# Optimization experiments

Hardware: AMD Instinct MI355X
Metric: run time of the kernel (lower is better)

Reference implementation:

```python
import jax, jax.numpy as jnp
import numpy as np
from jax import lax

EPS = 1e-10

def _ln(x, g, b):
    m = x.mean(-1, keepdims=True)
    v = x.var(-1, keepdims=True)
    return (x - m) / jnp.sqrt(v + 1e-5) * g + b

def _gather(t, idx):
    # t: (B, HW, c), idx: (B, HW, d) -> (B, HW, d, c); out[n,i,k,:] = t[n, idx[n,i,k], :]
    return jax.vmap(lambda tn, In: tn[In])(t, idx)

def setup_inputs() -> dict:
    key = jax.random.key(0)
    ks = jax.random.split(key, 20)
    b, v, c, d, h, w, hid, ksz = 2, 2, 128, 64, 64, 64, 256, 5
    hw = h * w
    Bf = b * v  # v_1 == 1 target view per reference view
    std = 0.02
    return {
        'features_mv': jax.random.normal(ks[0], (b, v, c, h, w), jnp.float32),
        'warp_indices': jax.random.randint(ks[1], (Bf, hw, d), 0, hw, jnp.int32),
        'depth_prob': jax.random.uniform(ks[2], (Bf, hw, d), jnp.float32),
        'ln1_g': jnp.ones((c,), jnp.float32), 'ln1_b': jnp.zeros((c,), jnp.float32),
        'wq': jax.random.normal(ks[3], (c, c), jnp.float32) * std, 'bq': jnp.zeros((c,), jnp.float32),
        'wk': jax.random.normal(ks[4], (c, c), jnp.float32) * std, 'bk': jnp.zeros((c,), jnp.float32),
        'wv': jax.random.normal(ks[5], (c, c), jnp.float32) * std, 'bv': jnp.zeros((c,), jnp.float32),
        'k_pe': jax.random.normal(ks[6], (1, 1, d), jnp.float32) * std,
        'v_pe': jax.random.normal(ks[7], (1, 1, d), jnp.float32) * std,
        'rpe': jax.random.normal(ks[8], (1, 1, d), jnp.float32) * std,
        'proj_w': jax.random.normal(ks[9], (c, c), jnp.float32) * std, 'proj_b': jnp.zeros((c,), jnp.float32),
        'ln2_g': jnp.ones((c,), jnp.float32), 'ln2_b': jnp.zeros((c,), jnp.float32),
        'fc1_w': jax.random.normal(ks[10], (c, hid), jnp.float32) * std, 'fc1_b': jnp.zeros((hid,), jnp.float32),
        'dw_w': jax.random.normal(ks[11], (hid, 1, ksz, ksz), jnp.float32) * std, 'dw_b': jnp.zeros((hid,), jnp.float32),
        'fc2_w': jax.random.normal(ks[12], (hid, c), jnp.float32) * std, 'fc2_b': jnp.zeros((c,), jnp.float32),
    }

def reference(features_mv, warp_indices, depth_prob, ln1_g, ln1_b, wq, bq, wk, bk, wv, bv,
              k_pe, v_pe, rpe, proj_w, proj_b, ln2_g, ln2_b, fc1_w, fc1_b, dw_w, dw_b, fc2_w, fc2_b):
    b, v, c, h, w = features_mv.shape
    hw = h * w
    hid = fc1_w.shape[1]
    scale = c ** (-0.5)  # num_heads = 1 -> head_dim = dim

    # (b v) (h w) c
    x = features_mv.reshape(b * v, c, hw).transpose(0, 2, 1)
    shortcut = x
    xn = _ln(x, ln1_g, ln1_b)
    q = xn @ wq + bq
    k = xn @ wk + bk
    vv = xn @ wv + bv

    # nn pairing: v=2, v_1=1 -> each reference view attends the other view
    Q = (q.reshape(b, v, hw, c) * scale).reshape(b * v, hw, c)
    K = k.reshape(b, v, hw, c)[:, ::-1].reshape(b * v, hw, c)
    V = vv.reshape(b, v, hw, c)[:, ::-1].reshape(b * v, hw, c)

    # SMM_QmK: cost[n,i,k] = sum_c Q[n,i,c] * K[n, idx[n,i,k], c]
    Kg = _gather(K, warp_indices)                       # (B, hw, d, c)
    cost = jnp.einsum('bic,bikc->bik', Q, Kg)
    Q_pe = Q.sum(-1, keepdims=True)                     # (B, hw, 1)
    cost = cost + Q_pe * k_pe + rpe                     # broadcast (1,1,d)

    # (Sim_UNet similarity refinement omitted: UNetModel source unavailable; identity here)
    attn = jax.nn.softmax(cost, axis=-1)
    attn = attn * depth_prob
    attn = (attn + EPS) / (attn.sum(-1, keepdims=True) + EPS)

    # SMM_AmV: out[n,i,c] = sum_k attn[n,i,k] * V[n, idx[n,i,k], c]
    Vg = _gather(V, warp_indices)                       # (B, hw, d, c)
    out = jnp.einsum('bik,bikc->bic', attn, Vg)
    out = out + (attn * v_pe).sum(-1, keepdims=True)

    # projection + residual (v_1 == 1 so B == b*v)
    x = shortcut + (out @ proj_w + proj_b)

    # ConvFFN residual branch
    xn2 = _ln(x, ln2_g, ln2_b)
    y = jax.nn.gelu(xn2 @ fc1_w + fc1_b, approximate=False)
    yi = y.transpose(0, 2, 1).reshape(b * v, hid, h, w)
    yc = lax.conv_general_dilated(yi, dw_w, (1, 1), 'SAME', feature_group_count=hid,
                                  dimension_numbers=('NCHW', 'OIHW', 'NCHW'))
    yc = jax.nn.gelu(yc + dw_b[None, :, None, None], approximate=False)
    y = y + yc.reshape(b * v, hid, hw).transpose(0, 2, 1)
    y = y @ fc2_w + fc2_b
    return x + y
```

## Files before the change

### kernel.cpp

```cpp
#include <hip/hip_runtime.h>
#include <math.h>

#define TOK   16384
#define HW    4096
#define C     128
#define D     64
#define HID   256

constexpr float LN_EPS = 1e-5f;
constexpr float EPS_R  = 1e-10f;
constexpr float QSCALE = 0.08838834764831845f;

typedef __attribute__((ext_vector_type(8))) short  bf16x8;
typedef __attribute__((ext_vector_type(4))) float  f32x4;
typedef __attribute__((ext_vector_type(2))) _Float16 half2v;
#define MFMA16(a, b, c) __builtin_amdgcn_mfma_f32_16x16x32_bf16((a), (b), (c), 0, 0, 0)

__device__ __forceinline__ float bflo(unsigned u) { return __uint_as_float(u << 16); }
__device__ __forceinline__ float bfhi(unsigned u) { return __uint_as_float(u & 0xffff0000u); }
__device__ __forceinline__ unsigned short f2bf(float f) {
  unsigned u = __float_as_uint(f);
  unsigned r = (u + 0x7fffu + ((u >> 16) & 1u)) >> 16;
  return (unsigned short)r;
}
__device__ __forceinline__ unsigned short f2h(float f) {
  _Float16 h = (_Float16)f;
  unsigned short r;
  __builtin_memcpy(&r, &h, 2);
  return r;
}
__device__ __forceinline__ float gelu_exact(float x) {
  return 0.5f * x * (1.0f + erff(x * 0.7071067811865476f));
}

union U4H { uint4 v; half2v h[4]; };
union U1H { unsigned v; half2v h; };

#if __has_builtin(__builtin_amdgcn_fdot2)
__device__ __forceinline__ float dot2h(half2v a, half2v b, float c) {
  return __builtin_amdgcn_fdot2(a, b, c, false);
}
#else
__device__ __forceinline__ float dot2h(half2v a, half2v b, float c) {
  return c + (float)a.x * (float)b.x + (float)a.y * (float)b.y;
}
#endif

__global__ __launch_bounds__(256) void k_prepln1(const float* __restrict__ wq,
    const float* __restrict__ wk, const float* __restrict__ wv,
    const float* __restrict__ pw, const float* __restrict__ f1w,
    const float* __restrict__ f2w, unsigned short* __restrict__ wt,
    const float* __restrict__ feat, const float* __restrict__ g,
    const float* __restrict__ b, unsigned short* __restrict__ xnb) {
  __shared__ float tile[32][C + 1];
  int bidx = blockIdx.x;
  if (bidx < 512) {
    int id = bidx * 256 + threadIdx.x;
    if (id < 16384) {
      int n = id >> 7, k = id & 127;
      wt[id] = f2bf(wq[k * 128 + n]);
    } else if (id < 32768) {
      int e = id - 16384; int n = e >> 7, k = e & 127;
      wt[id] = f2bf(wk[k * 128 + n]);
    } else if (id < 49152) {
      int e = id - 32768; int n = e >> 7, k = e & 127;
      wt[id] = f2bf(wv[k * 128 + n]);
    } else if (id < 65536) {
      int e = id - 49152; int n = e >> 7, k = e & 127;
      wt[id] = f2bf(pw[k * 128 + n]);
    } else if (id < 98304) {
      int e = id - 65536; int n = e >> 7, k = e & 127;
      wt[id] = f2bf(f1w[k * 256 + n]);
    } else {
      int e = id - 98304; int n = e >> 8, k = e & 255;
      wt[id] = f2bf(f2w[k * 128 + n]);
    }
    return;
  }
  int t0 = (bidx - 512) * 32;
  int n = t0 / HW, i0 = t0 % HW;
  int tid = threadIdx.x;
  const float* fb = feat + (size_t)n * C * HW;
  for (int e = tid; e < 32 * C; e += 256) {
    int ch = e >> 5, ii = e & 31;
    tile[ii][ch] = fb[(size_t)ch * HW + i0 + ii];
  }
  __syncthreads();
  int wave = tid >> 6, lane = tid & 63;
  for (int tkn = wave; tkn < 32; tkn += 4) {
    float a0 = tile[tkn][lane];
    float a1 = tile[tkn][lane + 64];
    float s = a0 + a1;
    for (int off = 32; off; off >>= 1) s += __shfl_xor(s, off, 64);
    float mean = s * (1.0f / 128.0f);
    float d0 = a0 - mean, d1 = a1 - mean;
    float v = d0 * d0 + d1 * d1;
    for (int off = 32; off; off >>= 1) v += __shfl_xor(v, off, 64);
    float rstd = rsqrtf(v * (1.0f / 128.0f) + LN_EPS);
    size_t ro = (size_t)(t0 + tkn) * C;
    xnb[ro + lane]      = f2bf(d0 * rstd * g[lane] + b[lane]);
    xnb[ro + lane + 64] = f2bf(d1 * rstd * g[lane + 64] + b[lane + 64]);
  }
}

__global__ __launch_bounds__(256) void k_qkv(const unsigned short* __restrict__ xnb,
    const unsigned short* __restrict__ wt,
    const float* __restrict__ bq, const float* __restrict__ bk,
    const float* __restrict__ bv, unsigned short* __restrict__ qh,
    unsigned short* __restrict__ ksw, unsigned short* __restrict__ vsw) {
  int w = threadIdx.x >> 6, lane = threadIdx.x & 63;
  int q4 = lane >> 4, m = lane & 15;
  int t0 = blockIdx.x * 64 + w * 16;
  int wsel = blockIdx.y >> 1;
  int hf = blockIdx.y & 1;
  const unsigned short* Wt = wt + wsel * 16384;
  const unsigned short* ap = xnb + (size_t)(t0 + m) * C + q4 * 8;
  bf16x8 a[4];
  #pragma unroll
  for (int ks = 0; ks < 4; ks++) a[ks] = *(const bf16x8*)(ap + ks * 32);
  f32x4 acc[4];
  #pragma unroll
  for (int nt = 0; nt < 4; nt++) acc[nt] = (f32x4){0.f, 0.f, 0.f, 0.f};
  #pragma unroll
  for (int nt = 0; nt < 4; nt++) {
    const unsigned short* bp = Wt + (size_t)(hf * 64 + nt * 16 + m) * C + q4 * 8;
    #pragma unroll
    for (int ks = 0; ks < 4; ks++) {
      bf16x8 bfrag = *(const bf16x8*)(bp + ks * 32);
      acc[nt] = MFMA16(a[ks], bfrag, acc[nt]);
    }
  }
  const float* B = (wsel == 0) ? bq : ((wsel == 1) ? bk : bv);
  float sc = (wsel == 0) ? QSCALE : 1.0f;
  unsigned short* O = (wsel == 0) ? qh : ((wsel == 1) ? ksw : vsw);
  int n = t0 >> 12, i0 = t0 & 4095;
  int base = (wsel == 0) ? t0 : (((n ^ 1) << 12) + i0);
  #pragma unroll
  for (int nt = 0; nt < 4; nt++) {
    int col = hf * 64 + nt * 16 + m;
    float bb = B[col];
    #pragma unroll
    for (int reg = 0; reg < 4; reg++) {
      int row = base + q4 * 4 + reg;
      O[(size_t)row * C + col] = f2h((acc[nt][reg] + bb) * sc);
    }
  }
}

__global__ __launch_bounds__(256, 3) void k_attn_proj_fc1(
    const unsigned short* __restrict__ qh, const unsigned short* __restrict__ ksw,
    const unsigned short* __restrict__ vsw, const int* __restrict__ widx,
    const float* __restrict__ dprob, const float* __restrict__ kpe,
    const float* __restrict__ vpe, const float* __restrict__ rpe,
    const unsigned short* __restrict__ wt, const float* __restrict__ pb,
    const float* __restrict__ feat, float* __restrict__ xio,
    const float* __restrict__ g2, const float* __restrict__ b2,
    const float* __restrict__ f1b, unsigned short* __restrict__ y) {
  __shared__ unsigned short axn[16 * C];
  __shared__ float ps1[4][16];
  __shared__ float ps2[4][16];
  int lane = threadIdx.x & 63;
  int wave = threadIdx.x >> 6;
  int bid = blockIdx.x;
  int n = (bid >> 1) & 3;
  int within = ((bid >> 3) << 1) | (bid & 1);
  int T0 = n * HW + within * 16;
  const unsigned short* Kb = ksw + (size_t)n * HW * C;
  const unsigned short* Vb = vsw + (size_t)n * HW * C;
  int gg = lane >> 3, s = lane & 7;
  half2v ones = {(_Float16)1.0f, (_Float16)1.0f};

  for (int tj = 0; tj < 4; ++tj) {
    int token = T0 + wave * 4 + tj;
    int myidx = widx[(size_t)token * D + lane];
    float mydp = dprob[(size_t)token * D + lane];
    half2v qreg[8];
    {
      const unsigned short* qp = qh + (size_t)token * C + s * 16;
      U4H qa, qb2;
      qa.v = *(const uint4*)(qp);
      qb2.v = *(const uint4*)(qp + 8);
      #pragma unroll
      for (int i = 0; i < 4; i++) { qreg[i] = qa.h[i]; qreg[4 + i] = qb2.h[i]; }
    }
    int rowv[8];
    #pragma unroll
    for (int pass = 0; pass < 8; ++pass)
      rowv[pass] = __shfl(myidx, pass * 8 + gg, 64);
    uint4 ka[8], kb[8];
    #pragma unroll
    for (int pass = 0; pass < 8; ++pass) {
      const unsigned short* kr = Kb + (size_t)rowv[pass] * C + s * 16;
      ka[pass] = *(const uint4*)(kr);
      kb[pass] = *(const uint4*)(kr + 8);
    }
    unsigned vv0[32];
    #pragma unroll
    for (int j = 0; j < 32; j++) {
      int row = __builtin_amdgcn_readlane(myidx, j);
      vv0[j] = *(const unsigned*)(Vb + (size_t)row * C + lane * 2);
    }
    float qpe = 0.f;
    #pragma unroll
    for (int i = 0; i < 8; i++) qpe = dot2h(qreg[i], ones, qpe);
    qpe += __shfl_xor(qpe, 1, 64);
    qpe += __shfl_xor(qpe, 2, 64);
    qpe += __shfl_xor(qpe, 4, 64);
    float mycost = 0.f;
    #pragma unroll
    for (int pass = 0; pass < 8; ++pass) {
      U4H ua, ub;
      ua.v = ka[pass]; ub.v = kb[pass];
      float p = 0.f;
      #pragma unroll
      for (int i = 0; i < 4; i++) p = dot2h(ua.h[i], qreg[i], p);
      #pragma unroll
      for (int i = 0; i < 4; i++) p = dot2h(ub.h[i], qreg[4 + i], p);
      p += __shfl_xor(p, 1, 64);
      p += __shfl_xor(p, 2, 64);
      p += __shfl_xor(p, 4, 64);
      float t = __shfl(p, (lane & 7) << 3, 64);
      if (pass == gg) mycost = t;
    }
    mycost += qpe * kpe[lane] + rpe[lane];
    float mx = mycost;
    for (int off = 32; off; off >>= 1) mx = fmaxf(mx, __shfl_xor(mx, off, 64));
    float e = __expf(mycost - mx);
    float ssum = e;
    for (int off = 32; off; off >>= 1) ssum += __shfl_xor(ssum, off, 64);
    float attn = (e / ssum) * mydp;
    float s2 = attn;
    for (int off = 32; off; off >>= 1) s2 += __shfl_xor(s2, off, 64);
    attn = (attn + EPS_R) / (s2 + EPS_R);
    float vpt = attn * vpe[lane];
    for (int off = 32; off; off >>= 1) vpt += __shfl_xor(vpt, off, 64);
    float o0 = vpt, o1 = vpt;
    unsigned att_u = __float_as_uint(attn);
    unsigned vv1[32];
    #pragma unroll
    for (int j = 0; j < 32; j++) {
      int row = __builtin_amdgcn_readlane(myidx, 32 + j);
      vv1[j] = *(const unsigned*)(Vb + (size_t)row * C + lane * 2);
    }
    #pragma unroll
    for (int j = 0; j < 32; j++) {
      float a = __uint_as_float(__builtin_amdgcn_readlane(att_u, j));
      U1H h; h.v = vv0[j];
      o0 += a * (float)h.h.x;
      o1 += a * (float)h.h.y;
    }
    #pragma unroll
    for (int j = 0; j < 32; j++) {
      float a = __uint_as_float(__builtin_amdgcn_readlane(att_u, 32 + j));
      U1H h; h.v = vv1[j];
      o0 += a * (float)h.h.x;
      o1 += a * (float)h.h.y;
    }
    unsigned pk = (unsigned)f2bf(o0) | ((unsigned)f2bf(o1) << 16);
    int row = wave * 4 + tj;
    int boff = row * 256 + lane * 4;
    boff ^= (row & 15) << 4;
    *(unsigned*)((char*)axn + boff) = pk;
  }
  __syncthreads();

  int q4 = lane >> 4, m = lane & 15;
  bf16x8 a[4];
  #pragma unroll
  for (int ks = 0; ks < 4; ks++) {
    int boff = m * 256 + ks * 64 + q4 * 16;
    boff ^= m << 4;
    a[ks] = *(const bf16x8*)((char*)axn + boff);
  }
  const unsigned short* Wp = wt + 3 * 16384;
  f32x4 acc[2];
  #pragma unroll
  for (int nt = 0; nt < 2; nt++) acc[nt] = (f32x4){0.f, 0.f, 0.f, 0.f};
  #pragma unroll
  for (int nt = 0; nt < 2; nt++) {
    int colt = wave * 32 + nt * 16;
    const unsigned short* bp = Wp + (size_t)(colt + m) * C + q4 * 8;
    #pragma unroll
    for (int ks = 0; ks < 4; ks++) {
      bf16x8 bfrag = *(const bf16x8*)(bp + ks * 32);
      acc[nt] = MFMA16(a[ks], bfrag, acc[nt]);
    }
  }
  int ibase = (T0 & 4095) + q4 * 4;
  float s1[4] = {0.f, 0.f, 0.f, 0.f}, s2b[4] = {0.f, 0.f, 0.f, 0.f};
  #pragma unroll
  for (int nt = 0; nt < 2; nt++) {
    int col = wave * 32 + nt * 16 + m;
    float bb = pb[col];
    const float* fp = feat + ((size_t)n * C + col) * HW + ibase;
    #pragma unroll
    for (int reg = 0; reg < 4; reg++) {
      float v = acc[nt][reg] + bb + fp[reg];
      acc[nt][reg] = v;
      s1[reg] += v;
      s2b[reg] += v * v;
    }
  }
  #pragma unroll
  for (int reg = 0; reg < 4; reg++) {
    #pragma unroll
    for (int off = 1; off < 16; off <<= 1) {
      s1[reg] += __shfl_xor(s1[reg], off, 64);
      s2b[reg] += __shfl_xor(s2b[reg], off, 64);
    }
  }
  if (m == 0) {
    #pragma unroll
    for (int reg = 0; reg < 4; reg++) {
      ps1[wave][q4 * 4 + reg] = s1[reg];
      ps2[wave][q4 * 4 + reg] = s2b[reg];
    }
  }
  __syncthreads();
  float mean[4], rstd[4];
  #pragma unroll
  for (int reg = 0; reg < 4; reg++) {
    int row = q4 * 4 + reg;
    float t1 = ps1[0][row] + ps1[1][row] + ps1[2][row] + ps1[3][row];
    float t2 = ps2[0][row] + ps2[1][row] + ps2[2][row] + ps2[3][row];
    mean[reg] = t1 * (1.0f / 128.0f);
    float var = t2 * (1.0f / 128.0f) - mean[reg] * mean[reg];
    rstd[reg] = rsqrtf(var + LN_EPS);
  }
  #pragma unroll
  for (int nt = 0; nt < 2; nt++) {
    int col = wave * 32 + nt * 16 + m;
    float gc = g2[col], bc = b2[col];
    #pragma unroll
    for (int reg = 0; reg < 4; reg++) {
      int row = q4 * 4 + reg;
      float v = acc[nt][reg];
      xio[(size_t)(T0 + row) * C + col] = v;
      unsigned short xv = f2bf((v - mean[reg]) * rstd[reg] * gc + bc);
      int boff = row * 256 + col * 2;
      boff ^= (row & 15) << 4;
      *(unsigned short*)((char*)axn + boff) = xv;
    }
  }
  __syncthreads();

  bf16x8 af[4];
  #pragma unroll
  for (int ks = 0; ks < 4; ks++) {
    int boff = m * 256 + ks * 64 + q4 * 16;
    boff ^= m << 4;
    af[ks] = *(const bf16x8*)((char*)axn + boff);
  }
  const unsigned short* Wf = wt + 65536;
  f32x4 acc2[4];
  #pragma unroll
  for (int nt = 0; nt < 4; nt++) acc2[nt] = (f32x4){0.f, 0.f, 0.f, 0.f};
  #pragma unroll
  for (int nt = 0; nt < 4; nt++) {
    int colt = wave * 64 + nt * 16;
    const unsigned short* bp = Wf + (size_t)(colt + m) * C + q4 * 8;
    #pragma unroll
    for (int ks = 0; ks < 4; ks++) {
      bf16x8 bfrag = *(const bf16x8*)(bp + ks * 32);
      acc2[nt] = MFMA16(af[ks], bfrag, acc2[nt]);
    }
  }
  #pragma unroll
  for (int nt = 0; nt < 4; nt++) {
    int col = wave * 64 + nt * 16 + m;
    float bb = f1b[col];
    #pragma unroll
    for (int reg = 0; reg < 4; reg++) {
      int row = T0 + q4 * 4 + reg;
      y[(size_t)row * HID + col] = f2bf(gelu_exact(acc2[nt][reg] + bb));
    }
  }
}

__global__ __launch_bounds__(256) void k_dwconv(const unsigned short* __restrict__ y,
    const float* __restrict__ w, const float* __restrict__ bias,
    unsigned short* __restrict__ ysum) {
  __shared__ float tile[8][401];
  __shared__ float wl[8][25];
  __shared__ float bl[8];
  __shared__ unsigned short outl[256][8];
  int bid = blockIdx.x;
  int tile_id = bid & 15;
  int cb = (bid >> 4) & 31;
  int n = bid >> 9;
  int ty = (tile_id >> 2) * 16, tx = (tile_id & 3) * 16;
  int ch0 = cb * 8;
  int tid = threadIdx.x;
  if (tid < 200) wl[tid / 25][tid % 25] = w[(size_t)(ch0 + tid / 25) * 25 + tid % 25];
  if (tid < 8) bl[tid] = bias[ch0 + tid];
  const unsigned short* yb = y + (size_t)n * HW * HID;
  for (int p = tid; p < 400; p += 256) {
    int py = p / 20, px = p % 20;
    int gy = ty + py - 2, gx = tx + px - 2;
    uint4 v = make_uint4(0u, 0u, 0u, 0u);
    if (gy >= 0 && gy < 64 && gx >= 0 && gx < 64)
      v = *(const uint4*)(yb + (size_t)(gy * 64 + gx) * HID + ch0);
    tile[0][p] = bflo(v.x); tile[1][p] = bfhi(v.x);
    tile[2][p] = bflo(v.y); tile[3][p] = bfhi(v.y);
    tile[4][p] = bflo(v.z); tile[5][p] = bfhi(v.z);
    tile[6][p] = bflo(v.w); tile[7][p] = bfhi(v.w);
  }
  __syncthreads();
  int cc = tid & 7;
  int xx = (tid >> 3) & 15;
  int yg = tid >> 7;
  float wreg[25];
  #pragma unroll
  for (int k = 0; k < 25; k++) wreg[k] = wl[cc][k];
  float bb = bl[cc];
  float win[12][5];
  #pragma unroll
  for (int r = 0; r < 12; r++)
    #pragma unroll
    for (int dx = 0; dx < 5; dx++)
      win[r][dx] = tile[cc][(yg * 8 + r) * 20 + xx + dx];
  #pragma unroll
  for (int j = 0; j < 8; ++j) {
    float acc = 0.f;
    #pragma unroll
    for (int dy = 0; dy < 5; ++dy)
      #pragma unroll
      for (int dx = 0; dx < 5; ++dx)
        acc += wreg[dy * 5 + dx] * win[j + dy][dx];
    float o = win[j + 2][2] + gelu_exact(acc + bb);
    int yy = yg * 8 + j;
    outl[yy * 16 + xx][cc] = f2bf(o);
  }
  __syncthreads();
  {
    int p = tid;
    int yy = p >> 4, xx2 = p & 15;
    uint4 val = *(const uint4*)outl[p];
    *(uint4*)(ysum + (size_t)(n * HW + (ty + yy) * 64 + tx + xx2) * HID + ch0) = val;
  }
}

__global__ __launch_bounds__(256) void k_fc2(const unsigned short* __restrict__ ysum,
    const unsigned short* __restrict__ wt, const float* __restrict__ f2b,
    const float* __restrict__ xio, float* __restrict__ outp) {
  int w = threadIdx.x >> 6, lane = threadIdx.x & 63;
  int q4 = lane >> 4, m = lane & 15;
  int t0 = blockIdx.x * 64 + w * 16;
  int quarter = blockIdx.y;
  const unsigned short* Wt = wt + 98304;
  const unsigned short* ap = ysum + (size_t)(t0 + m) * HID + q4 * 8;
  bf16x8 a[8];
  #pragma unroll
  for (int ks = 0; ks < 8; ks++) a[ks] = *(const bf16x8*)(ap + ks * 32);
  f32x4 acc[2];
  #pragma unroll
  for (int nt = 0; nt < 2; nt++) acc[nt] = (f32x4){0.f, 0.f, 0.f, 0.f};
  #pragma unroll
  for (int nt = 0; nt < 2; nt++) {
    const unsigned short* bp = Wt + (size_t)(quarter * 32 + nt * 16 + m) * HID + q4 * 8;
    #pragma unroll
    for (int ks = 0; ks < 8; ks++) {
      bf16x8 bfrag = *(const bf16x8*)(bp + ks * 32);
      acc[nt] = MFMA16(a[ks], bfrag, acc[nt]);
    }
  }
  #pragma unroll
  for (int nt = 0; nt < 2; nt++) {
    int col = quarter * 32 + nt * 16 + m;
    float bb = f2b[col];
    #pragma unroll
    for (int reg = 0; reg < 4; reg++) {
      int row = t0 + q4 * 4 + reg;
      outp[(size_t)row * C + col] = acc[nt][reg] + bb + xio[(size_t)row * C + col];
    }
  }
}

extern "C" void kernel_launch(void* const* d_in, const int* in_sizes, int n_in,
                              void* d_out, int out_size, void* d_ws, size_t ws_size,
                              hipStream_t stream) {
  (void)in_sizes; (void)n_in; (void)out_size; (void)ws_size;
  const float* feat  = (const float*)d_in[0];
  const int*   widx  = (const int*)d_in[1];
  const float* dprob = (const float*)d_in[2];
  const float* ln1g  = (const float*)d_in[3];
  const float* ln1b  = (const float*)d_in[4];
  const float* wq    = (const float*)d_in[5];
  const float* bq    = (const float*)d_in[6];
  const float* wk    = (const float*)d_in[7];
  const float* bk    = (const float*)d_in[8];
  const float* wv    = (const float*)d_in[9];
  const float* bv    = (const float*)d_in[10];
  const float* kpe   = (const float*)d_in[11];
  const float* vpe   = (const float*)d_in[12];
  const float* rpe   = (const float*)d_in[13];
  const float* pw    = (const float*)d_in[14];
  const float* pb    = (const float*)d_in[15];
  const float* ln2g  = (const float*)d_in[16];
  const float* ln2b  = (const float*)d_in[17];
  const float* f1w   = (const float*)d_in[18];
  const float* f1b   = (const float*)d_in[19];
  const float* dww   = (const float*)d_in[20];
  const float* dwb   = (const float*)d_in[21];
  const float* f2w   = (const float*)d_in[22];
  const float* f2b   = (const float*)d_in[23];

  float* ws = (float*)d_ws;
  const size_t M2 = (size_t)TOK * C;
  float* xio = ws;
  unsigned short* qhb   = (unsigned short*)(ws + M2);
  unsigned short* xnb   = (unsigned short*)(ws + M2 + M2 / 2);
  unsigned short* ksb   = (unsigned short*)(ws + 2 * M2);
  unsigned short* vsb   = (unsigned short*)(ws + 2 * M2 + M2 / 2);
  unsigned short* yb    = (unsigned short*)(ws + 3 * M2);
  unsigned short* ysumb = (unsigned short*)(ws + 4 * M2);
  unsigned short* wtb   = (unsigned short*)(ws + 5 * M2);

  k_prepln1<<<1024, 256, 0, stream>>>(wq, wk, wv, pw, f1w, f2w, wtb,
                                      feat, ln1g, ln1b, xnb);
  k_qkv    <<<dim3(TOK / 64, 6), 256, 0, stream>>>(xnb, wtb, bq, bk, bv, qhb, ksb, vsb);
  k_attn_proj_fc1<<<TOK / 16, 256, 0, stream>>>(qhb, ksb, vsb, widx, dprob, kpe, vpe,
                                                rpe, wtb, pb, feat, xio, ln2g, ln2b,
                                                f1b, yb);
  k_dwconv <<<2048, 256, 0, stream>>>(yb, dww, dwb, ysumb);
  k_fc2    <<<dim3(TOK / 64, 4), 256, 0, stream>>>(ysumb, wtb, f2b, xio, (float*)d_out);
}
```

Measured before the change: 201.2 us.

## Fuse LayerNorm1 into QKV projection and widen attention blocks to 512 threads

Splits the weight-prep kernel from LayerNorm1 and fuses LayerNorm1 directly into the QKV GEMM. Each 16-token block normalizes into a swizzled shared-memory tile and computes all three projections there, so the bf16 normalized intermediate is no longer written to and re-read from global memory. The attention/proj/fc1 kernel now uses 512-thread blocks: eight waves each handle two tokens, and the projection and fc1 column work is split eight ways. The QKV GEMM now runs with only 1024 blocks of 16 tokens, and the larger attention blocks may change occupancy and register pressure.

```diff
diff --git a/kernel.cpp b/kernel.cpp
--- a/kernel.cpp
+++ b/kernel.cpp
@@ -46,50 +46,53 @@
 }
 #endif
 
-__global__ __launch_bounds__(256) void k_prepln1(const float* __restrict__ wq,
+__global__ __launch_bounds__(256) void k_prep(const float* __restrict__ wq,
     const float* __restrict__ wk, const float* __restrict__ wv,
     const float* __restrict__ pw, const float* __restrict__ f1w,
-    const float* __restrict__ f2w, unsigned short* __restrict__ wt,
-    const float* __restrict__ feat, const float* __restrict__ g,
-    const float* __restrict__ b, unsigned short* __restrict__ xnb) {
-  __shared__ float tile[32][C + 1];
-  int bidx = blockIdx.x;
-  if (bidx < 512) {
-    int id = bidx * 256 + threadIdx.x;
-    if (id < 16384) {
-      int n = id >> 7, k = id & 127;
-      wt[id] = f2bf(wq[k * 128 + n]);
-    } else if (id < 32768) {
-      int e = id - 16384; int n = e >> 7, k = e & 127;
-      wt[id] = f2bf(wk[k * 128 + n]);
-    } else if (id < 49152) {
-      int e = id - 32768; int n = e >> 7, k = e & 127;
-      wt[id] = f2bf(wv[k * 128 + n]);
-    } else if (id < 65536) {
-      int e = id - 49152; int n = e >> 7, k = e & 127;
-      wt[id] = f2bf(pw[k * 128 + n]);
-    } else if (id < 98304) {
-      int e = id - 65536; int n = e >> 7, k = e & 127;
-      wt[id] = f2bf(f1w[k * 256 + n]);
-    } else {
-      int e = id - 98304; int n = e >> 8, k = e & 255;
-      wt[id] = f2bf(f2w[k * 128 + n]);
-    }
-    return;
-  }
-  int t0 = (bidx - 512) * 32;
-  int n = t0 / HW, i0 = t0 % HW;
+    const float* __restrict__ f2w, unsigned short* __restrict__ wt) {
+  int id = blockIdx.x * 256 + threadIdx.x;
+  if (id < 16384) {
+    int n = id >> 7, k = id & 127;
+    wt[id] = f2bf(wq[k * 128 + n]);
+  } else if (id < 32768) {
+    int e = id - 16384; int n = e >> 7, k = e & 127;
+    wt[id] = f2bf(wk[k * 128 + n]);
+  } else if (id < 49152) {
+    int e = id - 32768; int n = e >> 7, k = e & 127;
+    wt[id] = f2bf(wv[k * 128 + n]);
+  } else if (id < 65536) {
+    int e = id - 49152; int n = e >> 7, k = e & 127;
+    wt[id] = f2bf(pw[k * 128 + n]);
+  } else if (id < 98304) {
+    int e = id - 65536; int n = e >> 7, k = e & 127;
+    wt[id] = f2bf(f1w[k * 256 + n]);
+  } else {
+    int e = id - 98304; int n = e >> 8, k = e & 255;
+    wt[id] = f2bf(f2w[k * 128 + n]);
+  }
+}
+
+__global__ __launch_bounds__(256) void k_ln1qkv(const float* __restrict__ feat,
+    const float* __restrict__ g, const float* __restrict__ b,
+    const unsigned short* __restrict__ wt,
+    const float* __restrict__ bq, const float* __restrict__ bk,
+    const float* __restrict__ bv, unsigned short* __restrict__ qh,
+    unsigned short* __restrict__ ksw, unsigned short* __restrict__ vsw) {
+  __shared__ float t16[16][C + 1];
+  __shared__ unsigned short axn[16 * C];
   int tid = threadIdx.x;
-  const float* fb = feat + (size_t)n * C * HW;
-  for (int e = tid; e < 32 * C; e += 256) {
-    int ch = e >> 5, ii = e & 31;
-    tile[ii][ch] = fb[(size_t)ch * HW + i0 + ii];
-  }
-  __syncthreads();
-  int wave = tid >> 6, lane = tid & 63;
-  for (int tkn = wave; tkn < 32; tkn += 4) {
-    float a0 = tile[tkn][lane];
-    float a1 = tile[tkn][lane + 64];
+  int lane = tid & 63, wave = tid >> 6;
+  int t0 = blockIdx.x * 16;
+  int nv = t0 >> 12, i0 = t0 & 4095;
+  const float* fb = feat + (size_t)nv * C * HW;
+  for (int e = tid; e < 16 * C; e += 256) {
+    int ch = e >> 4, ii = e & 15;
+    t16[ii][ch] = fb[(size_t)ch * HW + i0 + ii];
+  }
+  __syncthreads();
+  for (int tkn = wave; tkn < 16; tkn += 4) {
+    float a0 = t16[tkn][lane];
+    float a1 = t16[tkn][lane + 64];
     float s = a0 + a1;
     for (int off = 32; off; off >>= 1) s += __shfl_xor(s, off, 64);
     float mean = s * (1.0f / 128.0f);
@@ -97,57 +100,48 @@
     float v = d0 * d0 + d1 * d1;
     for (int off = 32; off; off >>= 1) v += __shfl_xor(v, off, 64);
     float rstd = rsqrtf(v * (1.0f / 128.0f) + LN_EPS);
-    size_t ro = (size_t)(t0 + tkn) * C;
-    xnb[ro + lane]      = f2bf(d0 * rstd * g[lane] + b[lane]);
-    xnb[ro + lane + 64] = f2bf(d1 * rstd * g[lane + 64] + b[lane + 64]);
-  }
-}
-
-__global__ __launch_bounds__(256) void k_qkv(const unsigned short* __restrict__ xnb,
-    const unsigned short* __restrict__ wt,
-    const float* __restrict__ bq, const float* __restrict__ bk,
-    const float* __restrict__ bv, unsigned short* __restrict__ qh,
-    unsigned short* __restrict__ ksw, unsigned short* __restrict__ vsw) {
-  int w = threadIdx.x >> 6, lane = threadIdx.x & 63;
+    unsigned short x0 = f2bf(d0 * rstd * g[lane] + b[lane]);
+    unsigned short x1 = f2bf(d1 * rstd * g[lane + 64] + b[lane + 64]);
+    int b0 = (tkn * 256 + lane * 2) ^ ((tkn & 15) << 4);
+    int b1 = (tkn * 256 + (lane + 64) * 2) ^ ((tkn & 15) << 4);
+    *(unsigned short*)((char*)axn + b0) = x0;
+    *(unsigned short*)((char*)axn + b1) = x1;
+  }
+  __syncthreads();
   int q4 = lane >> 4, m = lane & 15;
-  int t0 = blockIdx.x * 64 + w * 16;
-  int wsel = blockIdx.y >> 1;
-  int hf = blockIdx.y & 1;
-  const unsigned short* Wt = wt + wsel * 16384;
-  const unsigned short* ap = xnb + (size_t)(t0 + m) * C + q4 * 8;
   bf16x8 a[4];
   #pragma unroll
-  for (int ks = 0; ks < 4; ks++) a[ks] = *(const bf16x8*)(ap + ks * 32);
-  f32x4 acc[4];
-  #pragma unroll
-  for (int nt = 0; nt < 4; nt++) acc[nt] = (f32x4){0.f, 0.f, 0.f, 0.f};
-  #pragma unroll
-  for (int nt = 0; nt < 4; nt++) {
-    const unsigned short* bp = Wt + (size_t)(hf * 64 + nt * 16 + m) * C + q4 * 8;
+  for (int ks = 0; ks < 4; ks++) {
+    int boff = (m * 256 + ks * 64 + q4 * 16) ^ (m << 4);
+    a[ks] = *(const bf16x8*)((char*)axn + boff);
+  }
+  int swbase = ((nv ^ 1) << 12) + i0;
+  #pragma unroll
+  for (int tt = 0; tt < 6; ++tt) {
+    int gt = wave * 6 + tt;
+    int mat = gt >> 3, ct = gt & 7;
+    const unsigned short* bp = wt + mat * 16384 + (size_t)(ct * 16 + m) * C + q4 * 8;
+    f32x4 acc = (f32x4){0.f, 0.f, 0.f, 0.f};
     #pragma unroll
     for (int ks = 0; ks < 4; ks++) {
       bf16x8 bfrag = *(const bf16x8*)(bp + ks * 32);
-      acc[nt] = MFMA16(a[ks], bfrag, acc[nt]);
-    }
-  }
-  const float* B = (wsel == 0) ? bq : ((wsel == 1) ? bk : bv);
-  float sc = (wsel == 0) ? QSCALE : 1.0f;
-  unsigned short* O = (wsel == 0) ? qh : ((wsel == 1) ? ksw : vsw);
-  int n = t0 >> 12, i0 = t0 & 4095;
-  int base = (wsel == 0) ? t0 : (((n ^ 1) << 12) + i0);
-  #pragma unroll
-  for (int nt = 0; nt < 4; nt++) {
-    int col = hf * 64 + nt * 16 + m;
+      acc = MFMA16(a[ks], bfrag, acc);
+    }
+    const float* B = (mat == 0) ? bq : ((mat == 1) ? bk : bv);
+    float sc = (mat == 0) ? QSCALE : 1.0f;
+    unsigned short* O = (mat == 0) ? qh : ((mat == 1) ? ksw : vsw);
+    int base = (mat == 0) ? t0 : swbase;
+    int col = ct * 16 + m;
     float bb = B[col];
     #pragma unroll
     for (int reg = 0; reg < 4; reg++) {
       int row = base + q4 * 4 + reg;
-      O[(size_t)row * C + col] = f2h((acc[nt][reg] + bb) * sc);
-    }
-  }
-}
-
-__global__ __launch_bounds__(256, 3) void k_attn_proj_fc1(
+      O[(size_t)row * C + col] = f2h((acc[reg] + bb) * sc);
+    }
+  }
+}
+
+__global__ __launch_bounds__(512, 4) void k_attn_proj_fc1(
     const unsigned short* __restrict__ qh, const unsigned short* __restrict__ ksw,
     const unsigned short* __restrict__ vsw, const int* __restrict__ widx,
     const float* __restrict__ dprob, const float* __restrict__ kpe,
@@ -157,8 +151,8 @@
     const float* __restrict__ g2, const float* __restrict__ b2,
     const float* __restrict__ f1b, unsigned short* __restrict__ y) {
   __shared__ unsigned short axn[16 * C];
-  __shared__ float ps1[4][16];
-  __shared__ float ps2[4][16];
+  __shared__ float ps1[8][16];
+  __shared__ float ps2[8][16];
   int lane = threadIdx.x & 63;
   int wave = threadIdx.x >> 6;
   int bid = blockIdx.x;
@@ -170,8 +164,8 @@
   int gg = lane >> 3, s = lane & 7;
   half2v ones = {(_Float16)1.0f, (_Float16)1.0f};
 
-  for (int tj = 0; tj < 4; ++tj) {
-    int token = T0 + wave * 4 + tj;
+  for (int tj = 0; tj < 2; ++tj) {
+    int token = T0 + wave * 2 + tj;
     int myidx = widx[(size_t)token * D + lane];
     float mydp = dprob[(size_t)token * D + lane];
     half2v qreg[8];
@@ -257,9 +251,8 @@
       o1 += a * (float)h.h.y;
     }
     unsigned pk = (unsigned)f2bf(o0) | ((unsigned)f2bf(o1) << 16);
-    int row = wave * 4 + tj;
-    int boff = row * 256 + lane * 4;
-    boff ^= (row & 15) << 4;
+    int row = wave * 2 + tj;
+    int boff = (row * 256 + lane * 4) ^ ((row & 15) << 4);
     *(unsigned*)((char*)axn + boff) = pk;
   }
   __syncthreads();
@@ -268,37 +261,31 @@
   bf16x8 a[4];
   #pragma unroll
   for (int ks = 0; ks < 4; ks++) {
-    int boff = m * 256 + ks * 64 + q4 * 16;
-    boff ^= m << 4;
+    int boff = (m * 256 + ks * 64 + q4 * 16) ^ (m << 4);
     a[ks] = *(const bf16x8*)((char*)axn + boff);
   }
   const unsigned short* Wp = wt + 3 * 16384;
-  f32x4 acc[2];
-  #pragma unroll
-  for (int nt = 0; nt < 2; nt++) acc[nt] = (f32x4){0.f, 0.f, 0.f, 0.f};
-  #pragma unroll
-  for (int nt = 0; nt < 2; nt++) {
-    int colt = wave * 32 + nt * 16;
-    const unsigned short* bp = Wp + (size_t)(colt + m) * C + q4 * 8;
+  f32x4 acc = (f32x4){0.f, 0.f, 0.f, 0.f};
+  {
+    const unsigned short* bp = Wp + (size_t)(wave * 16 + m) * C + q4 * 8;
     #pragma unroll
     for (int ks = 0; ks < 4; ks++) {
       bf16x8 bfrag = *(const bf16x8*)(bp + ks * 32);
-      acc[nt] = MFMA16(a[ks], bfrag, acc[nt]);
+      acc = MFMA16(a[ks], bfrag, acc);
     }
   }
   int ibase = (T0 & 4095) + q4 * 4;
-  float s1[4] = {0.f, 0.f, 0.f, 0.f}, s2b[4] = {0.f, 0.f, 0.f, 0.f};
-  #pragma unroll
-  for (int nt = 0; nt < 2; nt++) {
-    int col = wave * 32 + nt * 16 + m;
+  float s1[4], s2b[4];
+  {
+    int col = wave * 16 + m;
     float bb = pb[col];
     const float* fp = feat + ((size_t)n * C + col) * HW + ibase;
     #pragma unroll
     for (int reg = 0; reg < 4; reg++) {
-      float v = acc[nt][reg] + bb + fp[reg];
-      acc[nt][reg] = v;
-      s1[reg] += v;
-      s2b[reg] += v * v;
+      float v = acc[reg] + bb + fp[reg];
+      acc[reg] = v;
+      s1[reg] = v;
+      s2b[reg] = v * v;
     }
   }
   #pragma unroll
@@ -321,24 +308,23 @@
   #pragma unroll
   for (int reg = 0; reg < 4; reg++) {
     int row = q4 * 4 + reg;
-    float t1 = ps1[0][row] + ps1[1][row] + ps1[2][row] + ps1[3][row];
-    float t2 = ps2[0][row] + ps2[1][row] + ps2[2][row] + ps2[3][row];
+    float t1 = 0.f, t2 = 0.f;
+    #pragma unroll
+    for (int wv2 = 0; wv2 < 8; wv2++) { t1 += ps1[wv2][row]; t2 += ps2[wv2][row]; }
     mean[reg] = t1 * (1.0f / 128.0f);
     float var = t2 * (1.0f / 128.0f) - mean[reg] * mean[reg];
     rstd[reg] = rsqrtf(var + LN_EPS);
   }
-  #pragma unroll
-  for (int nt = 0; nt < 2; nt++) {
-    int col = wave * 32 + nt * 16 + m;
+  {
+    int col = wave * 16 + m;
     float gc = g2[col], bc = b2[col];
     #pragma unroll
     for (int reg = 0; reg < 4; reg++) {
       int row = q4 * 4 + reg;
-      float v = acc[nt][reg];
+      float v = acc[reg];
       xio[(size_t)(T0 + row) * C + col] = v;
       unsigned short xv = f2bf((v - mean[reg]) * rstd[reg] * gc + bc);
-      int boff = row * 256 + col * 2;
-      boff ^= (row & 15) << 4;
+      int boff = (row * 256 + col * 2) ^ ((row & 15) << 4);
       *(unsigned short*)((char*)axn + boff) = xv;
     }
   }
@@ -347,32 +333,26 @@
   bf16x8 af[4];
   #pragma unroll
   for (int ks = 0; ks < 4; ks++) {
-    int boff = m * 256 + ks * 64 + q4 * 16;
-    boff ^= m << 4;
+    int boff = (m * 256 + ks * 64 + q4 * 16) ^ (m << 4);
     af[ks] = *(const bf16x8*)((char*)axn + boff);
   }
   const unsigned short* Wf = wt + 65536;
-  f32x4 acc2[4];
-  #pragma unroll
-  for (int nt = 0; nt < 4; nt++) acc2[nt] = (f32x4){0.f, 0.f, 0.f, 0.f};
-  #pragma unroll
-  for (int nt = 0; nt < 4; nt++) {
-    int colt = wave * 64 + nt * 16;
+  #pragma unroll
+  for (int nt = 0; nt < 2; nt++) {
+    int colt = wave * 32 + nt * 16;
     const unsigned short* bp = Wf + (size_t)(colt + m) * C + q4 * 8;
+    f32x4 acc2 = (f32x4){0.f, 0.f, 0.f, 0.f};
     #pragma unroll
     for (int ks = 0; ks < 4; ks++) {
       bf16x8 bfrag = *(const bf16x8*)(bp + ks * 32);
-      acc2[nt] = MFMA16(af[ks], bfrag, acc2[nt]);
-    }
-  }
-  #pragma unroll
-  for (int nt = 0; nt < 4; nt++) {
-    int col = wave * 64 + nt * 16 + m;
+      acc2 = MFMA16(af[ks], bfrag, acc2);
+    }
+    int col = colt + m;
     float bb = f1b[col];
     #pragma unroll
     for (int reg = 0; reg < 4; reg++) {
       int row = T0 + q4 * 4 + reg;
-      y[(size_t)row * HID + col] = f2bf(gelu_exact(acc2[nt][reg] + bb));
+      y[(size_t)row * HID + col] = f2bf(gelu_exact(acc2[reg] + bb));
     }
   }
 }
@@ -509,19 +489,17 @@
   const size_t M2 = (size_t)TOK * C;
   float* xio = ws;
   unsigned short* qhb   = (unsigned short*)(ws + M2);
-  unsigned short* xnb   = (unsigned short*)(ws + M2 + M2 / 2);
   unsigned short* ksb   = (unsigned short*)(ws + 2 * M2);
   unsigned short* vsb   = (unsigned short*)(ws + 2 * M2 + M2 / 2);
   unsigned short* yb    = (unsigned short*)(ws + 3 * M2);
   unsigned short* ysumb = (unsigned short*)(ws + 4 * M2);
   unsigned short* wtb   = (unsigned short*)(ws + 5 * M2);
 
-  k_prepln1<<<1024, 256, 0, stream>>>(wq, wk, wv, pw, f1w, f2w, wtb,
-                                      feat, ln1g, ln1b, xnb);
-  k_qkv    <<<dim3(TOK / 64, 6), 256, 0, stream>>>(xnb, wtb, bq, bk, bv, qhb, ksb, vsb);
-  k_attn_proj_fc1<<<TOK / 16, 256, 0, stream>>>(qhb, ksb, vsb, widx, dprob, kpe, vpe,
-                                                rpe, wtb, pb, feat, xio, ln2g, ln2b,
-                                                f1b, yb);
+  k_prep   <<<512, 256, 0, stream>>>(wq, wk, wv, pw, f1w, f2w, wtb);
+  k_ln1qkv <<<1024, 256, 0, stream>>>(feat, ln1g, ln1b, wtb, bq, bk, bv, qhb, ksb, vsb);
+  k_attn_proj_fc1<<<1024, 512, 0, stream>>>(qhb, ksb, vsb, widx, dprob, kpe, vpe,
+                                            rpe, wtb, pb, feat, xio, ln2g, ln2b,
+                                            f1b, yb);
   k_dwconv <<<2048, 256, 0, stream>>>(yb, dww, dwb, ysumb);
   k_fc2    <<<dim3(TOK / 64, 4), 256, 0, stream>>>(ysumb, wtb, f2b, xio, (float*)d_out);
 }
```

After: 203.3 us. Within noise of the previous version (+1.0%).
